# Performance work log

Measured on AMD Instinct MI355X. Metric: run time of the kernel, lower is better.

Reference implementation:

```python
import jax, jax.numpy as jnp
import numpy as np

TEMPERATURE = 0.5
SCALE_LOSS = 1.0 / 32.0
LAMBDA = 0.0039


def setup_inputs() -> dict:
    key = jax.random.key(0)
    z = jax.random.normal(key, (4096, 6, 256), dtype=jnp.float32)
    return {"z": z}


def reference(z):
    B, V = z.shape[0], z.shape[1]
    # [B, V, ...] -> [V, B, D], L2-normalize embeddings
    zv = z.reshape(B, V, -1).transpose(1, 0, 2)
    zn = zv / jnp.linalg.norm(zv, axis=-1, keepdims=True)

    # Positive error: per-sample cross-view similarity [B, V, V]
    sim_pos = jnp.einsum('vbd,wbd->bvw', zn, zn)
    pos = jnp.exp((1.0 - sim_pos) / TEMPERATURE).mean(axis=(1, 2))  # [B]

    # Negative error: per-view within-batch similarity [V, B, B]
    sim_neg = jnp.exp(jnp.einsum('vbd,vcd->vbc', zn, zn) / TEMPERATURE)
    offdiag_mask = ~jnp.eye(B, dtype=bool)  # [B, B]
    off_mean = jnp.where(offdiag_mask[None], sim_neg, 0.0).sum(-1) / (B - 1)  # [V, B]
    neg = off_mean.sum(0)  # [B], accumulated over views

    return jnp.sum(pos) * SCALE_LOSS + LAMBDA * jnp.sum(neg)
```

## Files before the change

### kernel.cpp

```cpp
#include <hip/hip_runtime.h>
#include <cstdint>
#include <cstddef>

#define B_N 4096
#define V_N 6
#define D_N 256
#define NTILE 528
#define NBLK (NTILE * V_N)

typedef int i32x4 __attribute__((ext_vector_type(4)));

#define QC 298.0f
#define INV_C2_X2 (2.0f / (QC * QC))

__device__ __forceinline__ void async_load16(void* lds, const void* gmem) {
  __builtin_amdgcn_global_load_lds(
      (const __attribute__((address_space(1))) unsigned int*)gmem,
      (__attribute__((address_space(3))) unsigned int*)lds,
      16, 0, 0);
}

__global__ __launch_bounds__(256) void norm_pos_kernel(
    const float* __restrict__ z, signed char* __restrict__ znb,
    float* __restrict__ pos_part) {
  const int b = blockIdx.x;
  const int t = threadIdx.x;
  const int lane = t & 63;
  const int w = t >> 6;

  __shared__ float zs[V_N][D_N];
  __shared__ float red[V_N][4];
  __shared__ float inv[V_N];
  __shared__ float pred[4];

  const float* zb = z + (size_t)b * (V_N * D_N);
#pragma unroll
  for (int v = 0; v < V_N; ++v) zs[v][t] = zb[v * D_N + t];
  __syncthreads();

#pragma unroll
  for (int v = 0; v < V_N; ++v) {
    float x = zs[v][t];
    float s = x * x;
#pragma unroll
    for (int off = 32; off > 0; off >>= 1) s += __shfl_down(s, off);
    if (lane == 0) red[v][w] = s;
  }
  __syncthreads();
  if (t < V_N) inv[t] = rsqrtf(red[t][0] + red[t][1] + red[t][2] + red[t][3]);
  __syncthreads();

#pragma unroll
  for (int v = 0; v < V_N; ++v) {
    float q = rintf(zs[v][t] * inv[v] * QC);
    q = fminf(127.0f, fmaxf(-127.0f, q));
    znb[((size_t)v * B_N + b) * D_N + t] = (signed char)(int)q;
  }

  float psum = 0.0f;
  int pidx = 0;
#pragma unroll
  for (int v = 0; v < V_N; ++v) {
#pragma unroll
    for (int u = v + 1; u < V_N; ++u) {
      if ((pidx & 3) == w) {
        float s = 0.0f;
#pragma unroll
        for (int d = 0; d < D_N; d += 64) s += zs[v][lane + d] * zs[u][lane + d];
#pragma unroll
        for (int off = 32; off > 0; off >>= 1) s += __shfl_down(s, off);
        if (lane == 0) {
          float sim = s * inv[v] * inv[u];
          psum += __expf(2.0f * (1.0f - sim));
        }
      }
      ++pidx;
    }
  }
  if (lane == 0) pred[w] = psum;
  __syncthreads();
  if (t == 0) pos_part[b] = pred[0] + pred[1] + pred[2] + pred[3];
}

__global__ __launch_bounds__(256) void gram_kernel(
    const signed char* __restrict__ znb, float* __restrict__ neg_part) {
  const int v = blockIdx.y;
  const int t = blockIdx.x;
  int i = (int)((sqrtf(8.0f * (float)t + 1.0f) - 1.0f) * 0.5f);
  while ((i + 1) * (i + 2) / 2 <= t) ++i;
  while (i * (i + 1) / 2 > t) --i;
  const int j = t - i * (i + 1) / 2;

  const signed char* Zv = znb + (size_t)v * B_N * D_N;
  const signed char* Ag = Zv + (size_t)(i * 128) * D_N;
  const signed char* Bg = Zv + (size_t)(j * 128) * D_N;

  __shared__ signed char As[128][128];
  __shared__ signed char Bs[128][128];
  __shared__ float blk[4];

  const int tid = threadIdx.x;
  const int lane = tid & 63;
  const int w = tid >> 6;
  const int wr = w >> 1;
  const int wc = w & 1;

  i32x4 c[4][4];
#pragma unroll
  for (int a = 0; a < 4; ++a)
#pragma unroll
    for (int b2 = 0; b2 < 4; ++b2) c[a][b2] = (i32x4){0, 0, 0, 0};

  const int kc = lane >> 4;
  const int mrow = wr * 64 + (lane & 15);
  const int ncol = wc * 64 + (lane & 15);

  signed char* AsF = &As[0][0];
  signed char* BsF = &Bs[0][0];

  for (int k0 = 0; k0 < D_N; k0 += 128) {
    __syncthreads();
#pragma unroll
    for (int q = 0; q < 4; ++q) {
      const int s = tid + 256 * q;
      const int row = s >> 3;
      const int gc = (s & 7) ^ (row & 7);
      async_load16(AsF + s * 16, Ag + (size_t)row * D_N + k0 + gc * 16);
      async_load16(BsF + s * 16, Bg + (size_t)row * D_N + k0 + gc * 16);
    }
    __syncthreads();

#pragma unroll
    for (int kk = 0; kk < 2; ++kk) {
      const int cbase = kk * 4 + kc;
      i32x4 af[4], bfr[4];
#pragma unroll
      for (int f = 0; f < 4; ++f) {
        const int ra = mrow + 16 * f;
        const int rb2 = ncol + 16 * f;
        af[f]  = *(const i32x4*)(AsF + ra * 128 + ((cbase ^ (ra & 7)) * 16));
        bfr[f] = *(const i32x4*)(BsF + rb2 * 128 + ((cbase ^ (rb2 & 7)) * 16));
      }
#pragma unroll
      for (int fm = 0; fm < 4; ++fm)
#pragma unroll
        for (int fn = 0; fn < 4; ++fn)
          c[fm][fn] = __builtin_amdgcn_mfma_i32_16x16x64_i8(
              af[fm], bfr[fn], c[fm][fn], 0, 0, 0);
    }
  }

  float lsum = 0.0f;
  const int rb = i * 128 + wr * 64 + (lane >> 4) * 4;
  const int cb = j * 128 + wc * 64 + (lane & 15);
#pragma unroll
  for (int fm = 0; fm < 4; ++fm) {
#pragma unroll
    for (int fn = 0; fn < 4; ++fn) {
      const int gcol = cb + fn * 16;
#pragma unroll
      for (int r = 0; r < 4; ++r) {
        const int grow = rb + fm * 16 + r;
        float e = __expf((float)c[fm][fn][r] * INV_C2_X2);
        lsum += (grow == gcol) ? 0.0f : e;
      }
    }
  }
  if (i != j) lsum *= 2.0f;

#pragma unroll
  for (int off = 32; off > 0; off >>= 1) lsum += __shfl_down(lsum, off);
  if (lane == 0) blk[w] = lsum;
  __syncthreads();
  if (tid == 0) neg_part[t + NTILE * v] = blk[0] + blk[1] + blk[2] + blk[3];
}

__global__ __launch_bounds__(1024) void finalize_kernel(
    const float* __restrict__ pos_part, const float* __restrict__ neg_part,
    float* __restrict__ out) {
  const int t = threadIdx.x;
  const int lane = t & 63;
  const int w = t >> 6;
  __shared__ float pr[16], nr[16];

  float p = 0.0f;
  for (int idx = t; idx < B_N; idx += 1024) p += pos_part[idx];
  float n = 0.0f;
  for (int idx = t; idx < NBLK; idx += 1024) n += neg_part[idx];
#pragma unroll
  for (int off = 32; off > 0; off >>= 1) {
    p += __shfl_down(p, off);
    n += __shfl_down(n, off);
  }
  if (lane == 0) { pr[w] = p; nr[w] = n; }
  __syncthreads();
  if (t == 0) {
    float P = 0.0f, N = 0.0f;
#pragma unroll
    for (int k = 0; k < 16; ++k) { P += pr[k]; N += nr[k]; }
    out[0] = (1.0f / 32.0f) * ((float)B_N / 6.0f + P / 18.0f) +
             0.0039f * (N / (float)(B_N - 1));
  }
}

extern "C" void kernel_launch(void* const* d_in, const int* in_sizes, int n_in,
                              void* d_out, int out_size, void* d_ws, size_t ws_size,
                              hipStream_t stream) {
  const float* z = (const float*)d_in[0];
  float* out = (float*)d_out;
  float* pos_part = (float*)d_ws;
  float* neg_part = (float*)((char*)d_ws + 16384);
  signed char* znb = (signed char*)((char*)d_ws + 32768);

  norm_pos_kernel<<<B_N, 256, 0, stream>>>(z, znb, pos_part);
  dim3 grid(NTILE, V_N, 1);
  gram_kernel<<<grid, 256, 0, stream>>>(znb, neg_part);
  finalize_kernel<<<1, 1024, 0, stream>>>(pos_part, neg_part, out);
}
```

Measured before the change: 106.7 us.

## Rewrite norm/pos kernel to one wavefront per sample with register Gram

The normalize-and-positive kernel now assigns one 64-lane wavefront per batch sample instead of one 256-thread block. Each lane loads float4 values and computes all 21 view-pair partial dot products in registers, then reduces them with xor shuffles. This removes the LDS staging, the __syncthreads barriers and the duplicated per-pair reductions. It also packs the int8 quantized outputs into 32-bit stores. In exchange it uses more registers and runs 21 shuffle reductions per lane. This kernel is likely a small part of the total time, since the Gram kernel dominates.

```diff
diff --git a/kernel.cpp b/kernel.cpp
--- a/kernel.cpp
+++ b/kernel.cpp
@@ -23,63 +23,62 @@
 __global__ __launch_bounds__(256) void norm_pos_kernel(
     const float* __restrict__ z, signed char* __restrict__ znb,
     float* __restrict__ pos_part) {
-  const int b = blockIdx.x;
-  const int t = threadIdx.x;
-  const int lane = t & 63;
-  const int w = t >> 6;
-
-  __shared__ float zs[V_N][D_N];
-  __shared__ float red[V_N][4];
-  __shared__ float inv[V_N];
-  __shared__ float pred[4];
-
-  const float* zb = z + (size_t)b * (V_N * D_N);
-#pragma unroll
-  for (int v = 0; v < V_N; ++v) zs[v][t] = zb[v * D_N + t];
-  __syncthreads();
+  const int lane = threadIdx.x & 63;
+  const int w = threadIdx.x >> 6;
+  const int b = blockIdx.x * 4 + w;
+
+  const float4* zb4 = (const float4*)(z + (size_t)b * (V_N * D_N));
+  float4 x[V_N];
+#pragma unroll
+  for (int v = 0; v < V_N; ++v) x[v] = zb4[v * 64 + lane];
+
+  float s[21];
+  {
+    int p = 0;
+#pragma unroll
+    for (int v = 0; v < V_N; ++v)
+#pragma unroll
+      for (int u = v; u < V_N; ++u) {
+        s[p] = x[v].x * x[u].x + x[v].y * x[u].y +
+               x[v].z * x[u].z + x[v].w * x[u].w;
+        ++p;
+      }
+  }
+#pragma unroll
+  for (int off = 1; off < 64; off <<= 1)
+#pragma unroll
+    for (int q = 0; q < 21; ++q)
+      s[q] += __shfl_xor(s[q], off);
+
+  const int selfidx[V_N] = {0, 6, 11, 15, 18, 20};
+  float inv[V_N];
+#pragma unroll
+  for (int v = 0; v < V_N; ++v) inv[v] = rsqrtf(s[selfidx[v]]);
 
 #pragma unroll
   for (int v = 0; v < V_N; ++v) {
-    float x = zs[v][t];
-    float s = x * x;
-#pragma unroll
-    for (int off = 32; off > 0; off >>= 1) s += __shfl_down(s, off);
-    if (lane == 0) red[v][w] = s;
-  }
-  __syncthreads();
-  if (t < V_N) inv[t] = rsqrtf(red[t][0] + red[t][1] + red[t][2] + red[t][3]);
-  __syncthreads();
-
-#pragma unroll
-  for (int v = 0; v < V_N; ++v) {
-    float q = rintf(zs[v][t] * inv[v] * QC);
-    q = fminf(127.0f, fmaxf(-127.0f, q));
-    znb[((size_t)v * B_N + b) * D_N + t] = (signed char)(int)q;
+    const float sc = inv[v] * QC;
+    int q0 = (int)rintf(fminf(127.0f, fmaxf(-127.0f, x[v].x * sc)));
+    int q1 = (int)rintf(fminf(127.0f, fmaxf(-127.0f, x[v].y * sc)));
+    int q2 = (int)rintf(fminf(127.0f, fmaxf(-127.0f, x[v].z * sc)));
+    int q3 = (int)rintf(fminf(127.0f, fmaxf(-127.0f, x[v].w * sc)));
+    int packed = (q0 & 255) | ((q1 & 255) << 8) | ((q2 & 255) << 16)
+               | ((q3 & 255) << 24);
+    ((int*)(znb + ((size_t)v * B_N + b) * D_N))[lane] = packed;
   }
 
   float psum = 0.0f;
-  int pidx = 0;
-#pragma unroll
-  for (int v = 0; v < V_N; ++v) {
-#pragma unroll
-    for (int u = v + 1; u < V_N; ++u) {
-      if ((pidx & 3) == w) {
-        float s = 0.0f;
-#pragma unroll
-        for (int d = 0; d < D_N; d += 64) s += zs[v][lane + d] * zs[u][lane + d];
-#pragma unroll
-        for (int off = 32; off > 0; off >>= 1) s += __shfl_down(s, off);
-        if (lane == 0) {
-          float sim = s * inv[v] * inv[u];
-          psum += __expf(2.0f * (1.0f - sim));
-        }
-      }
-      ++pidx;
-    }
-  }
-  if (lane == 0) pred[w] = psum;
-  __syncthreads();
-  if (t == 0) pos_part[b] = pred[0] + pred[1] + pred[2] + pred[3];
+  {
+    int p = 0;
+#pragma unroll
+    for (int v = 0; v < V_N; ++v)
+#pragma unroll
+      for (int u = v; u < V_N; ++u) {
+        if (u > v) psum += __expf(2.0f * (1.0f - s[p] * inv[v] * inv[u]));
+        ++p;
+      }
+  }
+  if (lane == 0) pos_part[b] = psum;
 }
 
 __global__ __launch_bounds__(256) void gram_kernel(
@@ -212,7 +211,7 @@
   float* neg_part = (float*)((char*)d_ws + 16384);
   signed char* znb = (signed char*)((char*)d_ws + 32768);
 
-  norm_pos_kernel<<<B_N, 256, 0, stream>>>(z, znb, pos_part);
+  norm_pos_kernel<<<B_N / 4, 256, 0, stream>>>(z, znb, pos_part);
   dim3 grid(NTILE, V_N, 1);
   gram_kernel<<<grid, 256, 0, stream>>>(znb, neg_part);
   finalize_kernel<<<1, 1024, 0, stream>>>(pos_part, neg_part, out);
```

After: 100.4 us. 5.9% less time.
